# Optimization experiments

Hardware: AMD Instinct MI355X
Metric: run time of the kernel (lower is better)

The kernel has to match this reference:

```python
import jax, jax.numpy as jnp
import numpy as np

B, T, H, N = 16, 128, 8, 64
OUT_DIM = 64
EPS = 1e-8
LN_EPS = 1e-5  # torch LayerNorm default


def setup_inputs() -> dict:
    key = jax.random.key(0)
    k1, k2 = jax.random.split(key)
    sat_logits_seq = jax.random.normal(k1, (B, T, H, N, N), dtype=jnp.float32)
    ln_gamma = jnp.ones((N * 9,), dtype=jnp.float32)
    ln_beta = jnp.zeros((N * 9,), dtype=jnp.float32)
    W = jax.random.normal(k2, (N * 9, OUT_DIM), dtype=jnp.float32) * (1.0 / np.sqrt(N * 9))
    b = jnp.zeros((OUT_DIM,), dtype=jnp.float32)
    return {"sat_logits_seq": sat_logits_seq, "ln_gamma": ln_gamma,
            "ln_beta": ln_beta, "W": W, "b": b}


def reference(sat_logits_seq, ln_gamma, ln_beta, W, b):
    Bm, Tm, Hm, Nm, _ = sat_logits_seq.shape
    P = jax.nn.softmax(sat_logits_seq, axis=-1)              # (B,T,H,N,N)

    # 1) attention entropy per node, averaged over heads -> (B,T,N)
    pc = jnp.clip(P, EPS, None)
    ent = -(pc * jnp.log(pc)).sum(axis=-1).mean(axis=2)
    ent_mean = ent.mean(axis=1)
    ent_std = ent.std(axis=1)                                # unbiased=False (ddof=0)
    ent_range = ent.max(axis=1) - ent.min(axis=1)
    ent_slope = (ent[:, -1, :] - ent[:, 0, :]) / max(1, Tm - 1)

    # 2) distribution change rate (T > 1 here) -> (B,T-1,N)
    diff = jnp.abs(P[:, 1:] - P[:, :-1]).sum(axis=-1).mean(axis=2)
    diff_mean = diff.mean(axis=1)
    diff_std = diff.std(axis=1)
    diff_max = diff.max(axis=1)

    # 3) self-loop probability -> (B,T,N)
    diag = jnp.diagonal(P, axis1=3, axis2=4).mean(axis=2)
    diag_mean = diag.mean(axis=1)
    diag_std = diag.std(axis=1)

    feat_nodes = jnp.stack([ent_mean, ent_std, ent_range, ent_slope,
                            diff_mean, diff_std, diff_max,
                            diag_mean, diag_std], axis=-1)   # (B,N,9)
    feat = feat_nodes.reshape(Bm, Nm * 9)

    # proj: LayerNorm -> Linear -> ReLU (dropout = identity in eval)
    mu = feat.mean(axis=-1, keepdims=True)
    var = feat.var(axis=-1, keepdims=True)
    x = (feat - mu) * jax.lax.rsqrt(var + LN_EPS) * ln_gamma + ln_beta
    emb = jax.nn.relu(x @ W + b)
    return emb
```

## Files before the change

### kernel.cpp

```cpp
#include <hip/hip_runtime.h>
#include <hip/hip_bf16.h>
#include <math.h>

#define B_ 16
#define T_ 128
#define H_ 8
#define N_ 64
#define NCHUNK 8
#define CHUNK (T_ / NCHUNK)
#define NUNITS (B_ * N_ * NCHUNK)

#define K_ENT 4.0f
#define K_DIF 0.75f

template <int CTRL>
__device__ __forceinline__ float dpp_xadd(float x) {
  const int yi = __builtin_amdgcn_update_dpp(
      __float_as_int(x), __float_as_int(x), CTRL, 0xf, 0xf, false);
  return x + __int_as_float(yi);
}
template <int IMM>
__device__ __forceinline__ float swz_xadd(float x) {
  return x + __int_as_float(
                 __builtin_amdgcn_ds_swizzle(__float_as_int(x), IMM));
}
__device__ __forceinline__ float qsum(float x) {
  x = dpp_xadd<0xB1>(x);
  x = dpp_xadd<0x4E>(x);
  x = swz_xadd<0x101F>(x);
  return x;
}
__device__ __forceinline__ float hsum(float x) {
  x = dpp_xadd<0x128>(x);
  x = swz_xadd<0x401F>(x);
  x += __shfl_xor(x, 32, 64);
  return x;
}
__device__ __forceinline__ float fsum(float x) {
  x = dpp_xadd<0xB1>(x);
  x = dpp_xadd<0x4E>(x);
  x = swz_xadd<0x101F>(x);
  x = dpp_xadd<0x128>(x);
  x = swz_xadd<0x401F>(x);
  x += __shfl_xor(x, 32, 64);
  return x;
}

__global__ __launch_bounds__(256) void feat_partial_kernel(
    const float* __restrict__ sat, float* __restrict__ part) {
  const int wave = threadIdx.x >> 6;
  const int lane = threadIdx.x & 63;
  const int unit = blockIdx.x * 4 + wave;
  const int c = unit >> 10;
  const int bn = unit & 1023;
  const int b = bn >> 6;
  const int n = bn & 63;

  const int q = lane & 7;
  const int h = lane >> 3;

  const int t0 = c * CHUNK;

  const long long tstride = (long long)H_ * N_ * N_;
  const float* rowp = sat +
      ((((long long)(b * T_ + t0) * H_ + h) * N_ + n) * N_) + q * 4;

  const int cl = (n & 31) >> 2;
  const int ce = (n & 3) + ((n >= 32) ? 4 : 0);
  float msel[8];
#pragma unroll
  for (int j = 0; j < 8; ++j) msel[j] = (q == cl && j == ce) ? 1.f : 0.f;

  float prev[8];

  float ent_sum = 0.f, ent_s2 = 0.f, ent_max = -1e30f, ent_min = 1e30f;
  float ent_first = 0.f, ent_last = 0.f;
  float diff_sum = 0.f, diff_s2 = 0.f, diff_max = -1e30f;
  float diag_sum = 0.f, diag_s2 = 0.f;

  float4 ca0, ca1, cb0, cb1;

  ca0 = *(const float4*)(rowp);
  ca1 = *(const float4*)(rowp + 32);
  cb0 = *(const float4*)(rowp + tstride);
  cb1 = *(const float4*)(rowp + tstride + 32);

  if (c > 0) {
    const float* po = rowp - tstride;
    float4 o0 = *(const float4*)(po);
    float4 o1 = *(const float4*)(po + 32);
    float x[8] = {o0.x, o0.y, o0.z, o0.w, o1.x, o1.y, o1.z, o1.w};
    float e[8], s = 0.f;
#pragma unroll
    for (int j = 0; j < 8; ++j) {
      float ee = __expf(x[j]);
      e[j] = ee;
      s += ee;
    }
    s = qsum(s);
    const float inv = 1.0f / s;
#pragma unroll
    for (int j = 0; j < 8; ++j) prev[j] = e[j] * inv;
  } else {
#pragma unroll
    for (int j = 0; j < 8; ++j) prev[j] = 0.f;
  }
  rowp += 2 * tstride;

  for (int i = 0; i < 8; ++i) {
    float4 na0, na1, nb0, nb1;
    if (i < 7) {
      na0 = *(const float4*)(rowp);
      na1 = *(const float4*)(rowp + 32);
      nb0 = *(const float4*)(rowp + tstride);
      nb1 = *(const float4*)(rowp + tstride + 32);
      rowp += 2 * tstride;
    }

    float xa[8] = {ca0.x, ca0.y, ca0.z, ca0.w, ca1.x, ca1.y, ca1.z, ca1.w};
    float xb[8] = {cb0.x, cb0.y, cb0.z, cb0.w, cb1.x, cb1.y, cb1.z, cb1.w};

    float ea[8], eb[8];
    float sa = 0.f, da = 0.f, sb = 0.f, db = 0.f;
#pragma unroll
    for (int j = 0; j < 8; ++j) {
      const float eea = __expf(xa[j]), eeb = __expf(xb[j]);
      ea[j] = eea;
      eb[j] = eeb;
      sa += eea;
      da += eea * xa[j];
      sb += eeb;
      db += eeb * xb[j];
    }
    sa = qsum(sa);
    da = qsum(da);
    sb = qsum(sb);
    db = qsum(db);
    const float inva = 1.0f / sa, invb = 1.0f / sb;
    float ent_a = __logf(sa) - da * inva;
    float ent_b = __logf(sb) - db * invb;

    float dla = 0.f, dlb = 0.f, dga = 0.f, dgb = 0.f;
#pragma unroll
    for (int j = 0; j < 8; ++j) {
      const float pa = ea[j] * inva;
      const float pb = eb[j] * invb;
      dla += fabsf(pa - prev[j]);
      dlb += fabsf(pb - pa);
      dga = fmaf(pa, msel[j], dga);
      dgb = fmaf(pb, msel[j], dgb);
      prev[j] = pb;
    }

    dla = fsum(dla);
    dlb = fsum(dlb);
    ent_a = hsum(ent_a);
    ent_b = hsum(ent_b);
    dga = hsum(dga);
    dgb = hsum(dgb);

    ent_a *= 0.125f;
    ent_b *= 0.125f;
    dla *= 0.125f;
    dlb *= 0.125f;
    dga *= 0.125f;
    dgb *= 0.125f;

    const float za = ent_a - K_ENT, zb = ent_b - K_ENT;
    ent_sum += ent_a + ent_b;
    ent_s2 += za * za + zb * zb;
    ent_max = fmaxf(ent_max, fmaxf(ent_a, ent_b));
    ent_min = fminf(ent_min, fminf(ent_a, ent_b));
    if (!(c == 0 && i == 0)) {
      const float wa = dla - K_DIF;
      diff_sum += dla;
      diff_s2 += wa * wa;
      diff_max = fmaxf(diff_max, dla);
    }
    const float wb = dlb - K_DIF;
    diff_sum += dlb;
    diff_s2 += wb * wb;
    diff_max = fmaxf(diff_max, dlb);
    diag_sum += dga + dgb;
    diag_s2 += dga * dga + dgb * dgb;
    if (c == 0 && i == 0) ent_first = ent_a;
    if (c == NCHUNK - 1 && i == 7) ent_last = ent_b;

    ca0 = na0;
    ca1 = na1;
    cb0 = nb0;
    cb1 = nb1;
  }

  const float dsum = __shfl(diag_sum, cl, 64);
  const float ds2 = __shfl(diag_s2, cl, 64);

  if (lane == 0) {
    float* o = part + (size_t)((b * N_ + n) * NCHUNK + c) * 12;
    o[0] = ent_sum;  o[1] = ent_s2;  o[2] = ent_max;  o[3] = ent_min;
    o[4] = ent_first; o[5] = ent_last;
    o[6] = diff_sum; o[7] = diff_s2; o[8] = diff_max;
    o[9] = dsum;     o[10] = ds2;
  }
}

__global__ __launch_bounds__(256) void head_kernel(
    const float* __restrict__ part, const float* __restrict__ gamma,
    const float* __restrict__ beta, const float* __restrict__ W,
    const float* __restrict__ bias, float* __restrict__ out) {
  const int b = blockIdx.x;
  const int tid = threadIdx.x;
  const int lane = tid & 63;
  const int wv = tid >> 6;

  __shared__ float xn[N_ * 9];
  __shared__ float red[4][N_];

  if (wv == 0) {
    float ent_sum = 0.f, ent_s2 = 0.f, ent_max = -1e30f, ent_min = 1e30f;
    float ent_first = 0.f, ent_last = 0.f;
    float diff_sum = 0.f, diff_s2 = 0.f, diff_max = -1e30f;
    float diag_sum = 0.f, diag_s2 = 0.f;

    const float* base = part + ((size_t)b * N_ + lane) * NCHUNK * 12;
#pragma unroll
    for (int c = 0; c < NCHUNK; ++c) {
      const float* o = base + c * 12;
      ent_sum += o[0];
      ent_s2 += o[1];
      ent_max = fmaxf(ent_max, o[2]);
      ent_min = fminf(ent_min, o[3]);
      if (c == 0) ent_first = o[4];
      if (c == NCHUNK - 1) ent_last = o[5];
      diff_sum += o[6];
      diff_s2 += o[7];
      diff_max = fmaxf(diff_max, o[8]);
      diag_sum += o[9];
      diag_s2 += o[10];
    }

    float f[9];
    const float em = ent_sum * (1.f / 128.f);
    const float emz = em - K_ENT;
    f[0] = em;
    f[1] = sqrtf(fmaxf(ent_s2 * (1.f / 128.f) - emz * emz, 0.f));
    f[2] = ent_max - ent_min;
    f[3] = (ent_last - ent_first) * (1.f / 127.f);
    const float dm = diff_sum * (1.f / 127.f);
    const float dmz = dm - K_DIF;
    f[4] = dm;
    f[5] = sqrtf(fmaxf(diff_s2 * (1.f / 127.f) - dmz * dmz, 0.f));
    f[6] = diff_max;
    const float gm = diag_sum * (1.f / 128.f);
    f[7] = gm;
    f[8] = sqrtf(fmaxf(diag_s2 * (1.f / 128.f) - gm * gm, 0.f));

    float ls = 0.f;
#pragma unroll
    for (int k = 0; k < 9; ++k) ls += f[k];
#pragma unroll
    for (int w = 1; w < 64; w <<= 1) ls += __shfl_xor(ls, w, 64);
    const float mu = ls * (1.f / 576.f);

    float lv = 0.f;
#pragma unroll
    for (int k = 0; k < 9; ++k) {
      const float dd = f[k] - mu;
      lv += dd * dd;
    }
#pragma unroll
    for (int w = 1; w < 64; w <<= 1) lv += __shfl_xor(lv, w, 64);
    const float rstd = rsqrtf(lv * (1.f / 576.f) + 1e-5f);

#pragma unroll
    for (int k = 0; k < 9; ++k) {
      const int idx = lane * 9 + k;
      xn[idx] = (f[k] - mu) * rstd * gamma[idx] + beta[idx];
    }
  }
  __syncthreads();

  float acc = 0.f;
  const int k0 = wv * 144;
#pragma unroll 8
  for (int k = k0; k < k0 + 144; ++k) acc = fmaf(xn[k], W[k * 64 + lane], acc);
  red[wv][lane] = acc;
  __syncthreads();

  if (wv == 0) {
    const float r =
        red[0][lane] + red[1][lane] + red[2][lane] + red[3][lane] + bias[lane];
    out[b * 64 + lane] = fmaxf(r, 0.f);
  }
}

extern "C" void kernel_launch(void* const* d_in, const int* in_sizes, int n_in,
                              void* d_out, int out_size, void* d_ws,
                              size_t ws_size, hipStream_t stream) {
  const float* sat = (const float*)d_in[0];
  const float* gamma = (const float*)d_in[1];
  const float* beta = (const float*)d_in[2];
  const float* W = (const float*)d_in[3];
  const float* bias = (const float*)d_in[4];
  float* out = (float*)d_out;
  float* part = (float*)d_ws;

  feat_partial_kernel<<<NUNITS / 4, 256, 0, stream>>>(sat, part);
  head_kernel<<<B_, 256, 0, stream>>>(part, gamma, beta, W, bias, out);
}
```

Measured before the change: 60.64 us.

## Halve time chunks, use nontemporal loads, and set occupancy launch bound

Time is now split into 4 chunks of 32 steps per unit instead of 8 chunks of 16. This halves the grid size and the redundant reload of the boundary row before each chunk. All input loads become nontemporal vector loads, because the 33 MB input is streamed once. The kernel also asks for 4 blocks per CU via launch bounds. The cost is fewer waves in flight to hide memory latency, and nontemporal hints may change cache behaviour in ways that are hard to predict.

New measurement: 57.28 us, median of 2. 1.06x faster.

```diff
diff --git a/kernel.cpp b/kernel.cpp
--- a/kernel.cpp
+++ b/kernel.cpp
@@ -6,12 +6,19 @@
 #define T_ 128
 #define H_ 8
 #define N_ 64
-#define NCHUNK 8
+#define NCHUNK 4
 #define CHUNK (T_ / NCHUNK)
+#define NPAIR (CHUNK / 2)
 #define NUNITS (B_ * N_ * NCHUNK)
 
 #define K_ENT 4.0f
 #define K_DIF 0.75f
+
+typedef float f32x4 __attribute__((ext_vector_type(4)));
+
+__device__ __forceinline__ f32x4 ntload(const float* p) {
+  return __builtin_nontemporal_load((const f32x4*)p);
+}
 
 template <int CTRL>
 __device__ __forceinline__ float dpp_xadd(float x) {
@@ -46,7 +53,7 @@
   return x;
 }
 
-__global__ __launch_bounds__(256) void feat_partial_kernel(
+__global__ __launch_bounds__(256, 4) void feat_partial_kernel(
     const float* __restrict__ sat, float* __restrict__ part) {
   const int wave = threadIdx.x >> 6;
   const int lane = threadIdx.x & 63;
@@ -78,18 +85,18 @@
   float diff_sum = 0.f, diff_s2 = 0.f, diff_max = -1e30f;
   float diag_sum = 0.f, diag_s2 = 0.f;
 
-  float4 ca0, ca1, cb0, cb1;
-
-  ca0 = *(const float4*)(rowp);
-  ca1 = *(const float4*)(rowp + 32);
-  cb0 = *(const float4*)(rowp + tstride);
-  cb1 = *(const float4*)(rowp + tstride + 32);
+  f32x4 ca0, ca1, cb0, cb1;
+
+  ca0 = ntload(rowp);
+  ca1 = ntload(rowp + 32);
+  cb0 = ntload(rowp + tstride);
+  cb1 = ntload(rowp + tstride + 32);
 
   if (c > 0) {
     const float* po = rowp - tstride;
-    float4 o0 = *(const float4*)(po);
-    float4 o1 = *(const float4*)(po + 32);
-    float x[8] = {o0.x, o0.y, o0.z, o0.w, o1.x, o1.y, o1.z, o1.w};
+    f32x4 o0 = ntload(po);
+    f32x4 o1 = ntload(po + 32);
+    float x[8] = {o0[0], o0[1], o0[2], o0[3], o1[0], o1[1], o1[2], o1[3]};
     float e[8], s = 0.f;
 #pragma unroll
     for (int j = 0; j < 8; ++j) {
@@ -107,18 +114,18 @@
   }
   rowp += 2 * tstride;
 
-  for (int i = 0; i < 8; ++i) {
-    float4 na0, na1, nb0, nb1;
-    if (i < 7) {
-      na0 = *(const float4*)(rowp);
-      na1 = *(const float4*)(rowp + 32);
-      nb0 = *(const float4*)(rowp + tstride);
-      nb1 = *(const float4*)(rowp + tstride + 32);
+  for (int i = 0; i < NPAIR; ++i) {
+    f32x4 na0, na1, nb0, nb1;
+    if (i < NPAIR - 1) {
+      na0 = ntload(rowp);
+      na1 = ntload(rowp + 32);
+      nb0 = ntload(rowp + tstride);
+      nb1 = ntload(rowp + tstride + 32);
       rowp += 2 * tstride;
     }
 
-    float xa[8] = {ca0.x, ca0.y, ca0.z, ca0.w, ca1.x, ca1.y, ca1.z, ca1.w};
-    float xb[8] = {cb0.x, cb0.y, cb0.z, cb0.w, cb1.x, cb1.y, cb1.z, cb1.w};
+    float xa[8] = {ca0[0], ca0[1], ca0[2], ca0[3], ca1[0], ca1[1], ca1[2], ca1[3]};
+    float xb[8] = {cb0[0], cb0[1], cb0[2], cb0[3], cb1[0], cb1[1], cb1[2], cb1[3]};
 
     float ea[8], eb[8];
     float sa = 0.f, da = 0.f, sb = 0.f, db = 0.f;
@@ -184,7 +191,7 @@
     diag_sum += dga + dgb;
     diag_s2 += dga * dga + dgb * dgb;
     if (c == 0 && i == 0) ent_first = ent_a;
-    if (c == NCHUNK - 1 && i == 7) ent_last = ent_b;
+    if (c == NCHUNK - 1 && i == NPAIR - 1) ent_last = ent_b;
 
     ca0 = na0;
     ca1 = na1;
```
